# Kernel optimization log

Measured on AMD Instinct MI355X. Metric: run time of the kernel, lower is better.

The kernel has to match this reference:

```python
import jax, jax.numpy as jnp
import numpy as np

D = 512          # embedding_dim (cfg.hidden_size)
K = 1024         # codebook_size
DECAY = 0.99
EPS = 1e-05
COMMITMENT_COST = 0.25


def setup_inputs() -> dict:
    key = jax.random.key(0)
    k1, k2, k3 = jax.random.split(key, 3)
    return {
        "inputs": jax.random.normal(k1, (32, 1024, D), dtype=jnp.float32),
        "embedding_weight": jax.random.normal(k2, (K, D), dtype=jnp.float32),
        "ema_cluster_size": jnp.zeros((K,), dtype=jnp.float32),
        "ema_w": jax.random.normal(k3, (K, D), dtype=jnp.float32),
    }


def reference(inputs, embedding_weight, ema_cluster_size, ema_w):
    input_shape = inputs.shape
    flat = inputs.reshape(-1, D)  # [N, D]

    # Squared L2 distances to every codebook entry: [N, K]
    distances = (
        jnp.sum(flat ** 2, axis=1, keepdims=True)
        + jnp.sum(embedding_weight ** 2, axis=1)
        - 2.0 * flat @ embedding_weight.T
    )
    idx = jnp.argmin(distances, axis=1)                      # [N]
    encodings = jax.nn.one_hot(idx, K, dtype=flat.dtype)     # [N, K]

    # ---- EMA codebook update (training path) ----
    counts = jnp.sum(encodings, axis=0)                      # == bincount(idx)
    new_cs = ema_cluster_size * DECAY + (1.0 - DECAY) * counts
    n = jnp.sum(new_cs)
    new_cs = (new_cs + EPS) / (n + K * EPS) * n              # Laplace smoothing
    # dw = encodings.T @ flat, done as a fused gather-reduce instead of dense matmul
    dw = jax.ops.segment_sum(flat, idx, num_segments=K)      # [K, D]
    new_ema_w = ema_w * DECAY + (1.0 - DECAY) * dw
    new_embedding = new_ema_w / new_cs[:, None]              # updated codebook

    # quantized = encodings @ new_embedding, expressed as a gather
    quantized = new_embedding[idx].reshape(input_shape)

    e_latent_loss = jnp.mean((jax.lax.stop_gradient(quantized) - inputs) ** 2)
    loss = COMMITMENT_COST * e_latent_loss

    # straight-through estimator
    quantized = inputs + jax.lax.stop_gradient(quantized - inputs)

    avg_probs = jnp.mean(encodings, axis=0)
    perplexity = jnp.exp(-jnp.sum(avg_probs * jnp.log(avg_probs + 1e-10)))
    return (loss, quantized, perplexity, encodings)
```

## Files before the change

### kernel.cpp

```cpp
#include <hip/hip_runtime.h>

#define NROWS 32768
#define DIM   512
#define KC    1024

typedef __attribute__((ext_vector_type(8)))  short short8v;
typedef __attribute__((ext_vector_type(16))) float f32x16;

#define AS1 __attribute__((address_space(1)))
#define AS3 __attribute__((address_space(3)))

__global__ __launch_bounds__(256) void k_enorm(const float* __restrict__ E,
                                               float* __restrict__ en2) {
    int w = threadIdx.x >> 6, lane = threadIdx.x & 63;
    int c = blockIdx.x * 4 + w;
    const float* row = E + (size_t)c * DIM;
    float4 a = *reinterpret_cast<const float4*>(&row[lane * 8]);
    float4 b = *reinterpret_cast<const float4*>(&row[lane * 8 + 4]);
    float s = a.x*a.x + a.y*a.y + a.z*a.z + a.w*a.w
            + b.x*b.x + b.y*b.y + b.z*b.z + b.w*b.w;
    #pragma unroll
    for (int off = 32; off; off >>= 1) s += __shfl_xor(s, off);
    if (!lane) en2[c] = s;
}

__device__ __forceinline__ void split_bf16(float v, short& hi, short& lo) {
    unsigned u = __float_as_uint(v);
    unsigned r = u + 0x7FFFu + ((u >> 16) & 1u);
    hi = (short)(r >> 16);
    float hif = __uint_as_float(r & 0xFFFF0000u);
    float rem = v - hif;
    unsigned u2 = __float_as_uint(rem);
    unsigned r2 = u2 + 0x7FFFu + ((u2 >> 16) & 1u);
    lo = (short)(r2 >> 16);
}

__device__ __forceinline__ unsigned long long pack_key(float d, int c) {
    unsigned u = __float_as_uint(d);
    u = (u & 0x80000000u) ? ~u : (u | 0x80000000u);
    return ((unsigned long long)u << 32) | (unsigned)c;
}

__global__ __launch_bounds__(256) void k_split(const float* __restrict__ x,
                                               const float* __restrict__ E,
                                               short* __restrict__ xfrag,
                                               short* __restrict__ efrag,
                                               int* __restrict__ counts,
                                               unsigned long long* __restrict__ packed) {
    __shared__ short hbuf[32][520];
    __shared__ short lbuf[32][520];
    int b = blockIdx.x, t = threadIdx.x;
    const float* src;
    short* dst;
    if (b < NROWS / 32) {
        src = x + (size_t)b * 32 * DIM;
        dst = xfrag + (size_t)b * 32768;
        if (b == 0) {
            #pragma unroll
            for (int i = 0; i < 4; ++i) counts[t + i * 256] = 0;
        }
    } else {
        int eb = b - NROWS / 32;
        src = E + (size_t)eb * 32 * DIM;
        dst = efrag + (size_t)eb * 32768;
        unsigned long long* p = packed + eb * 1024;
        #pragma unroll
        for (int i = 0; i < 4; ++i) p[t + i * 256] = 0xFFFFFFFFFFFFFFFFull;
    }
    #pragma unroll
    for (int f = 0; f < 16; ++f) {
        int u = t + f * 256;
        int row = u >> 7, c4 = (u & 127) * 4;
        float4 v = *reinterpret_cast<const float4*>(&src[row * DIM + c4]);
        short4 h4, l4;
        split_bf16(v.x, h4.x, l4.x); split_bf16(v.y, h4.y, l4.y);
        split_bf16(v.z, h4.z, l4.z); split_bf16(v.w, h4.w, l4.w);
        *reinterpret_cast<short4*>(&hbuf[row][c4]) = h4;
        *reinterpret_cast<short4*>(&lbuf[row][c4]) = l4;
    }
    __syncthreads();
    #pragma unroll
    for (int f = 0; f < 16; ++f) {
        int u = t + f * 256;
        int lane = u & 63, h = (u >> 6) & 1, kb = u >> 7;
        int row = lane & 31, k0 = kb * 16 + (lane >> 5) * 8;
        const short* s = h ? &lbuf[row][k0] : &hbuf[row][k0];
        short8v val = *reinterpret_cast<const short8v*>(s);
        *reinterpret_cast<short8v*>(&dst[(size_t)u * 8]) = val;
    }
}

__global__ __launch_bounds__(256, 2) void k_argmin(const short* __restrict__ xfrag,
                                                   const short* __restrict__ efrag,
                                                   const float* __restrict__ en2,
                                                   unsigned long long* __restrict__ packed) {
    __shared__ short sbuf[3][12288];
    const int tid = threadIdx.x;
    const int w = tid >> 6, l = tid & 63;
    const int wr = w >> 1, wc = w & 1;
    const int l31 = l & 31, lh = l >> 5;

    int bid = blockIdx.x;
    int xcd = bid & 7, j = bid >> 3;
    int row0 = (xcd * 32 + (j >> 2)) * 128;
    int c0   = (j & 3) * 256;

    const short* gsrc[6];
    #pragma unroll
    for (int s = 0; s < 6; ++s) {
        int q = s * 4 + w, g = q >> 1, h = q & 1;
        const short* base = (g < 4)
            ? xfrag + (size_t)(row0 / 32 + g) * 32768
            : efrag + (size_t)(c0 / 32 + (g - 4)) * 32768;
        gsrc[s] = base + h * 512 + l * 8;
    }

    f32x16 acc[2][4];
    #pragma unroll
    for (int a = 0; a < 2; ++a)
        #pragma unroll
        for (int b = 0; b < 4; ++b)
            #pragma unroll
            for (int r = 0; r < 16; ++r) acc[a][b][r] = 0.f;

    #pragma unroll
    for (int s = 0; s < 6; ++s)
        __builtin_amdgcn_global_load_lds((const AS1 void*)gsrc[s],
                                         (AS3 void*)&sbuf[0][(s * 4 + w) * 512],
                                         16, 0, 0);
    #pragma unroll
    for (int s = 0; s < 6; ++s)
        __builtin_amdgcn_global_load_lds((const AS1 void*)(gsrc[s] + 1024),
                                         (AS3 void*)&sbuf[1][(s * 4 + w) * 512],
                                         16, 0, 0);
    asm volatile("s_waitcnt vmcnt(6)" ::: "memory");
    __builtin_amdgcn_s_barrier();

    #pragma unroll 3
    for (int kb = 0; kb < 30; ++kb) {
        const int cur = kb % 3, nxt = (kb + 2) % 3;
        #pragma unroll
        for (int s = 0; s < 6; ++s)
            __builtin_amdgcn_global_load_lds(
                (const AS1 void*)(gsrc[s] + (size_t)(kb + 2) * 1024),
                (AS3 void*)&sbuf[nxt][(s * 4 + w) * 512], 16, 0, 0);
        {
            short8v ah[2], al[2], bh[4], bl[4];
            const short* sb = sbuf[cur];
            #pragma unroll
            for (int m = 0; m < 2; ++m) {
                int g = wr * 2 + m;
                ah[m] = *reinterpret_cast<const short8v*>(&sb[(g * 2 + 0) * 512 + l * 8]);
                al[m] = *reinterpret_cast<const short8v*>(&sb[(g * 2 + 1) * 512 + l * 8]);
            }
            #pragma unroll
            for (int n = 0; n < 4; ++n) {
                int g = 4 + wc * 4 + n;
                bh[n] = *reinterpret_cast<const short8v*>(&sb[(g * 2 + 0) * 512 + l * 8]);
                bl[n] = *reinterpret_cast<const short8v*>(&sb[(g * 2 + 1) * 512 + l * 8]);
            }
            #pragma unroll
            for (int m = 0; m < 2; ++m)
                #pragma unroll
                for (int n = 0; n < 4; ++n) {
                    acc[m][n] = __builtin_amdgcn_mfma_f32_32x32x16_bf16(
                        ah[m], bh[n], acc[m][n], 0, 0, 0);
                    acc[m][n] = __builtin_amdgcn_mfma_f32_32x32x16_bf16(
                        ah[m], bl[n], acc[m][n], 0, 0, 0);
                    acc[m][n] = __builtin_amdgcn_mfma_f32_32x32x16_bf16(
                        al[m], bh[n], acc[m][n], 0, 0, 0);
                }
        }
        asm volatile("s_waitcnt vmcnt(6) lgkmcnt(0)" ::: "memory");
        __builtin_amdgcn_s_barrier();
    }

    #pragma unroll
    for (int e = 0; e < 2; ++e) {
        const int kb = 30 + e, cur = kb % 3;
        short8v ah[2], al[2], bh[4], bl[4];
        const short* sb = sbuf[cur];
        #pragma unroll
        for (int m = 0; m < 2; ++m) {
            int g = wr * 2 + m;
            ah[m] = *reinterpret_cast<const short8v*>(&sb[(g * 2 + 0) * 512 + l * 8]);
            al[m] = *reinterpret_cast<const short8v*>(&sb[(g * 2 + 1) * 512 + l * 8]);
        }
        #pragma unroll
        for (int n = 0; n < 4; ++n) {
            int g = 4 + wc * 4 + n;
            bh[n] = *reinterpret_cast<const short8v*>(&sb[(g * 2 + 0) * 512 + l * 8]);
            bl[n] = *reinterpret_cast<const short8v*>(&sb[(g * 2 + 1) * 512 + l * 8]);
        }
        #pragma unroll
        for (int m = 0; m < 2; ++m)
            #pragma unroll
            for (int n = 0; n < 4; ++n) {
                acc[m][n] = __builtin_amdgcn_mfma_f32_32x32x16_bf16(
                    ah[m], bh[n], acc[m][n], 0, 0, 0);
                acc[m][n] = __builtin_amdgcn_mfma_f32_32x32x16_bf16(
                    ah[m], bl[n], acc[m][n], 0, 0, 0);
                acc[m][n] = __builtin_amdgcn_mfma_f32_32x32x16_bf16(
                    al[m], bh[n], acc[m][n], 0, 0, 0);
            }
        if (e == 0) {
            asm volatile("s_waitcnt vmcnt(0) lgkmcnt(0)" ::: "memory");
            __builtin_amdgcn_s_barrier();
        }
    }

    float e2[4];
    #pragma unroll
    for (int n = 0; n < 4; ++n) e2[n] = en2[c0 + wc * 128 + n * 32 + l31];
    #pragma unroll
    for (int m = 0; m < 2; ++m) {
        #pragma unroll
        for (int r = 0; r < 16; ++r) {
            unsigned long long key = 0xFFFFFFFFFFFFFFFFull;
            #pragma unroll
            for (int n = 0; n < 4; ++n) {
                float d = fmaf(-2.f, acc[m][n][r], e2[n]);
                unsigned long long k = pack_key(d, c0 + wc * 128 + n * 32 + l31);
                if (k < key) key = k;
            }
            #pragma unroll
            for (int off = 1; off < 32; off <<= 1) {
                unsigned long long o = __shfl_xor(key, off);
                if (o < key) key = o;
            }
            if (l31 == 0) {
                int grow = row0 + wr * 64 + m * 32 + (r & 3) + 8 * (r >> 2) + 4 * lh;
                atomicMin(&packed[grow], key);
            }
        }
    }
}

__global__ __launch_bounds__(256) void k_hist(const unsigned long long* __restrict__ packed,
                                              int* __restrict__ idx,
                                              int* __restrict__ counts) {
    __shared__ int h[KC];
    for (int i = threadIdx.x; i < KC; i += 256) h[i] = 0;
    __syncthreads();
    int g = blockIdx.x * 256 + threadIdx.x;
    int c = (int)(unsigned)(packed[g] & 0xFFFFFFFFull);
    idx[g] = c;
    atomicAdd(&h[c], 1);
    __syncthreads();
    for (int i = threadIdx.x; i < KC; i += 256)
        if (h[i]) atomicAdd(&counts[i], h[i]);
}

__global__ __launch_bounds__(1024) void k_meta(const int* __restrict__ counts,
                                               const float* __restrict__ ema_cs,
                                               float* __restrict__ smoothed,
                                               int* __restrict__ offsets,
                                               int* __restrict__ cursor,
                                               float* __restrict__ perp_out) {
    __shared__ float ws1[16], ws2[16];
    __shared__ int wsum[16];
    int t = threadIdx.x, lane = t & 63, w = t >> 6;
    int cnt = counts[t];
    float cs = ema_cs[t] * 0.99f + 0.01f * (float)cnt;
    float p = (float)cnt / 32768.f;
    float v1 = cs, v2 = p * logf(p + 1e-10f);
    #pragma unroll
    for (int off = 32; off; off >>= 1) {
        v1 += __shfl_xor(v1, off);
        v2 += __shfl_xor(v2, off);
    }
    int s = cnt;
    #pragma unroll
    for (int off = 1; off < 64; off <<= 1) {
        int u = __shfl_up(s, off);
        if (lane >= off) s += u;
    }
    if (lane == 0) { ws1[w] = v1; ws2[w] = v2; }
    if (lane == 63) wsum[w] = s;
    __syncthreads();
    float n = 0.f;
    #pragma unroll
    for (int i = 0; i < 16; ++i) n += ws1[i];
    smoothed[t] = (cs + 1e-5f) / (n + 1024.f * 1e-5f) * n;
    if (t == 0) {
        float sp = 0.f;
        #pragma unroll
        for (int i = 0; i < 16; ++i) sp += ws2[i];
        perp_out[0] = expf(-sp);
    }
    int wo = 0;
    for (int i = 0; i < 16; ++i) if (i < w) wo += wsum[i];
    int off_ = wo + s - cnt;
    offsets[t] = off_;
    cursor[t] = off_;
}

__global__ __launch_bounds__(256) void k_scatter(const int* __restrict__ idx,
                                                 int* __restrict__ cursor,
                                                 int* __restrict__ bucket) {
    int g = blockIdx.x * 256 + threadIdx.x;
    int c = idx[g];
    int pos = atomicAdd(&cursor[c], 1);
    bucket[pos] = g;
}

__global__ __launch_bounds__(256) void k_dw(const float* __restrict__ x,
                                            const float* __restrict__ ema_w,
                                            const int* __restrict__ offsets,
                                            const int* __restrict__ counts,
                                            const int* __restrict__ bucket,
                                            const float* __restrict__ smoothed,
                                            float* __restrict__ newE) {
    __shared__ int rows[256];
    int k = blockIdx.x >> 1, half = blockIdx.x & 1, t = threadIdx.x;
    int d = half * 256 + t;
    int beg = offsets[k], m = counts[k];
    float a = 0.f;
    for (int base = 0; base < m; base += 256) {
        int n = min(256, m - base);
        __syncthreads();
        if (t < n) rows[t] = bucket[beg + base + t];
        __syncthreads();
        int i = 0;
        for (; i + 4 <= n; i += 4) {
            float v0 = x[(size_t)rows[i]     * DIM + d];
            float v1 = x[(size_t)rows[i + 1] * DIM + d];
            float v2 = x[(size_t)rows[i + 2] * DIM + d];
            float v3 = x[(size_t)rows[i + 3] * DIM + d];
            a += v0 + v1 + v2 + v3;
        }
        for (; i < n; ++i) a += x[(size_t)rows[i] * DIM + d];
    }
    newE[(size_t)k * DIM + d] =
        (ema_w[(size_t)k * DIM + d] * 0.99f + 0.01f * a) / smoothed[k];
}

__global__ __launch_bounds__(256) void k_qe(const float* __restrict__ x,
                                            const int* __restrict__ idx,
                                            const float* __restrict__ newE,
                                            float* __restrict__ outq,
                                            float* __restrict__ enc,
                                            float* __restrict__ partials) {
    int b = blockIdx.x, t = threadIdx.x;
    int row8 = b * 8;
    float lp = 0.f;
    #pragma unroll
    for (int it = 0; it < 4; ++it) {
        int slot = t + it * 256;
        int r = slot >> 7;
        int c4 = (slot & 127) * 4;
        int row = row8 + r;
        int code = idx[row];
        float4 in = *reinterpret_cast<const float4*>(&x[(size_t)row * DIM + c4]);
        float4 q  = *reinterpret_cast<const float4*>(&newE[(size_t)code * DIM + c4]);
        float4 d;
        d.x = q.x - in.x; d.y = q.y - in.y; d.z = q.z - in.z; d.w = q.w - in.w;
        float4 o;
        o.x = in.x + d.x; o.y = in.y + d.y; o.z = in.z + d.z; o.w = in.w + d.w;
        *reinterpret_cast<float4*>(&outq[(size_t)row * DIM + c4]) = o;
        lp += d.x*d.x + d.y*d.y + d.z*d.z + d.w*d.w;
    }
    {
        int er = row8 + (t >> 5);
        int l32 = t & 31;
        int one = idx[er];
        float4* dst = reinterpret_cast<float4*>(enc + (size_t)er * KC);
        #pragma unroll
        for (int s = 0; s < 8; ++s) {
            int c4 = l32 + s * 32;
            int base = c4 * 4;
            float4 v;
            v.x = (one == base)     ? 1.f : 0.f;
            v.y = (one == base + 1) ? 1.f : 0.f;
            v.z = (one == base + 2) ? 1.f : 0.f;
            v.w = (one == base + 3) ? 1.f : 0.f;
            dst[c4] = v;
        }
    }
    #pragma unroll
    for (int off = 32; off; off >>= 1) lp += __shfl_xor(lp, off);
    __shared__ float wr[4];
    int lane = t & 63, w = t >> 6;
    if (!lane) wr[w] = lp;
    __syncthreads();
    if (t == 0) partials[b] = wr[0] + wr[1] + wr[2] + wr[3];
}

__global__ __launch_bounds__(256) void k_lossfin(const float* __restrict__ partials,
                                                 float* __restrict__ out0) {
    __shared__ double red[256];
    double s = 0.0;
    for (int i = threadIdx.x; i < 4096; i += 256) s += (double)partials[i];
    red[threadIdx.x] = s; __syncthreads();
    for (int st = 128; st; st >>= 1) {
        if (threadIdx.x < st) red[threadIdx.x] += red[threadIdx.x + st];
        __syncthreads();
    }
    if (!threadIdx.x) out0[0] = (float)(0.25 * red[0] / 16777216.0);
}

extern "C" void kernel_launch(void* const* d_in, const int* in_sizes, int n_in,
                              void* d_out, int out_size, void* d_ws, size_t ws_size,
                              hipStream_t stream) {
    const float* x   = (const float*)d_in[0];
    const float* E   = (const float*)d_in[1];
    const float* ecs = (const float*)d_in[2];
    const float* emw = (const float*)d_in[3];
    float* out = (float*)d_out;

    char* ws = (char*)d_ws;
    int*   idx      = (int*)(ws + 0);
    int*   bucket   = (int*)(ws + 131072);
    float* en2      = (float*)(ws + 262144);
    int*   counts   = (int*)(ws + 266240);
    int*   offsets  = (int*)(ws + 270336);
    int*   cursor   = (int*)(ws + 274432);
    float* smoothed = (float*)(ws + 278528);
    float* newE     = (float*)(ws + 282624);
    float* partials = (float*)(ws + 282624 + 2097152);
    unsigned long long* packed = (unsigned long long*)newE;

    float* out_loss = out;
    float* out_q    = out + 1;
    float* out_perp = out + 16777217;
    float* out_enc  = out + 16777218;

    short* xfrag = (short*)out_enc;
    short* efrag = xfrag + (size_t)NROWS * DIM * 2;

    k_enorm  <<<KC / 4, 256, 0, stream>>>(E, en2);
    k_split  <<<NROWS / 32 + KC / 32, 256, 0, stream>>>(x, E, xfrag, efrag,
                                                        counts, packed);
    k_argmin <<<(NROWS / 128) * 4, 256, 0, stream>>>(xfrag, efrag, en2, packed);
    k_hist   <<<NROWS / 256, 256, 0, stream>>>(packed, idx, counts);
    k_meta   <<<1, 1024, 0, stream>>>(counts, ecs, smoothed, offsets, cursor, out_perp);
    k_scatter<<<NROWS / 256, 256, 0, stream>>>(idx, cursor, bucket);
    k_dw     <<<KC * 2, 256, 0, stream>>>(x, emw, offsets, counts, bucket, smoothed, newE);
    k_qe     <<<NROWS / 8, 256, 0, stream>>>(x, idx, newE, out_q, out_enc, partials);
    k_lossfin<<<1, 256, 0, stream>>>(partials, out_loss);
}
```

Before: 301.1 us.

## Fuse x bf16 split into argmin GEMM loop and merge E prep kernels

```diff
diff --git a/kernel.cpp b/kernel.cpp
--- a/kernel.cpp
+++ b/kernel.cpp
@@ -9,20 +9,6 @@
 
 #define AS1 __attribute__((address_space(1)))
 #define AS3 __attribute__((address_space(3)))
-
-__global__ __launch_bounds__(256) void k_enorm(const float* __restrict__ E,
-                                               float* __restrict__ en2) {
-    int w = threadIdx.x >> 6, lane = threadIdx.x & 63;
-    int c = blockIdx.x * 4 + w;
-    const float* row = E + (size_t)c * DIM;
-    float4 a = *reinterpret_cast<const float4*>(&row[lane * 8]);
-    float4 b = *reinterpret_cast<const float4*>(&row[lane * 8 + 4]);
-    float s = a.x*a.x + a.y*a.y + a.z*a.z + a.w*a.w
-            + b.x*b.x + b.y*b.y + b.z*b.z + b.w*b.w;
-    #pragma unroll
-    for (int off = 32; off; off >>= 1) s += __shfl_xor(s, off);
-    if (!lane) en2[c] = s;
-}
 
 __device__ __forceinline__ void split_bf16(float v, short& hi, short& lo) {
     unsigned u = __float_as_uint(v);
@@ -35,38 +21,44 @@
     lo = (short)(r2 >> 16);
 }
 
+__device__ __forceinline__ void conv8(const float4 a, const float4 b,
+                                      short8v& hi, short8v& lo) {
+    short h, l;
+    split_bf16(a.x, h, l); hi[0] = h; lo[0] = l;
+    split_bf16(a.y, h, l); hi[1] = h; lo[1] = l;
+    split_bf16(a.z, h, l); hi[2] = h; lo[2] = l;
+    split_bf16(a.w, h, l); hi[3] = h; lo[3] = l;
+    split_bf16(b.x, h, l); hi[4] = h; lo[4] = l;
+    split_bf16(b.y, h, l); hi[5] = h; lo[5] = l;
+    split_bf16(b.z, h, l); hi[6] = h; lo[6] = l;
+    split_bf16(b.w, h, l); hi[7] = h; lo[7] = l;
+}
+
 __device__ __forceinline__ unsigned long long pack_key(float d, int c) {
     unsigned u = __float_as_uint(d);
     u = (u & 0x80000000u) ? ~u : (u | 0x80000000u);
     return ((unsigned long long)u << 32) | (unsigned)c;
 }
 
-__global__ __launch_bounds__(256) void k_split(const float* __restrict__ x,
-                                               const float* __restrict__ E,
-                                               short* __restrict__ xfrag,
+__global__ __launch_bounds__(256) void k_eprep(const float* __restrict__ E,
                                                short* __restrict__ efrag,
+                                               float* __restrict__ en2,
                                                int* __restrict__ counts,
                                                unsigned long long* __restrict__ packed) {
     __shared__ short hbuf[32][520];
     __shared__ short lbuf[32][520];
     int b = blockIdx.x, t = threadIdx.x;
-    const float* src;
-    short* dst;
-    if (b < NROWS / 32) {
-        src = x + (size_t)b * 32 * DIM;
-        dst = xfrag + (size_t)b * 32768;
-        if (b == 0) {
-            #pragma unroll
-            for (int i = 0; i < 4; ++i) counts[t + i * 256] = 0;
-        }
-    } else {
-        int eb = b - NROWS / 32;
-        src = E + (size_t)eb * 32 * DIM;
-        dst = efrag + (size_t)eb * 32768;
-        unsigned long long* p = packed + eb * 1024;
-        #pragma unroll
-        for (int i = 0; i < 4; ++i) p[t + i * 256] = 0xFFFFFFFFFFFFFFFFull;
-    }
+    const float* src = E + (size_t)b * 32 * DIM;
+    short* dst = efrag + (size_t)b * 32768;
+
+    unsigned long long* p = packed + b * 1024;
+    #pragma unroll
+    for (int i = 0; i < 4; ++i) p[t + i * 256] = 0xFFFFFFFFFFFFFFFFull;
+    if (b == 0) {
+        #pragma unroll
+        for (int i = 0; i < 4; ++i) counts[t + i * 256] = 0;
+    }
+
     #pragma unroll
     for (int f = 0; f < 16; ++f) {
         int u = t + f * 256;
@@ -88,9 +80,22 @@
         short8v val = *reinterpret_cast<const short8v*>(s);
         *reinterpret_cast<short8v*>(&dst[(size_t)u * 8]) = val;
     }
-}
-
-__global__ __launch_bounds__(256, 2) void k_argmin(const short* __restrict__ xfrag,
+
+    int w = t >> 6, lane = t & 63;
+    for (int cc = 0; cc < 8; ++cc) {
+        int c = b * 32 + w * 8 + cc;
+        const float* row = E + (size_t)c * DIM;
+        float4 a = *reinterpret_cast<const float4*>(&row[lane * 8]);
+        float4 bb = *reinterpret_cast<const float4*>(&row[lane * 8 + 4]);
+        float s = a.x*a.x + a.y*a.y + a.z*a.z + a.w*a.w
+                + bb.x*bb.x + bb.y*bb.y + bb.z*bb.z + bb.w*bb.w;
+        #pragma unroll
+        for (int off = 32; off; off >>= 1) s += __shfl_xor(s, off);
+        if (!lane) en2[c] = s;
+    }
+}
+
+__global__ __launch_bounds__(256, 2) void k_argmin(const float* __restrict__ x,
                                                    const short* __restrict__ efrag,
                                                    const float* __restrict__ en2,
                                                    unsigned long long* __restrict__ packed) {
@@ -105,14 +110,12 @@
     int row0 = (xcd * 32 + (j >> 2)) * 128;
     int c0   = (j & 3) * 256;
 
-    const short* gsrc[6];
-    #pragma unroll
-    for (int s = 0; s < 6; ++s) {
-        int q = s * 4 + w, g = q >> 1, h = q & 1;
-        const short* base = (g < 4)
-            ? xfrag + (size_t)(row0 / 32 + g) * 32768
-            : efrag + (size_t)(c0 / 32 + (g - 4)) * 32768;
-        gsrc[s] = base + h * 512 + l * 8;
+    const float* axsrc = x + (size_t)(row0 + w * 32 + l31) * DIM + lh * 8;
+    const short* gsrc[4];
+    #pragma unroll
+    for (int s = 0; s < 4; ++s) {
+        int gb = w * 2 + (s >> 1), h = s & 1;
+        gsrc[s] = efrag + (size_t)(c0 / 32 + gb) * 32768 + h * 512 + l * 8;
     }
 
     f32x16 acc[2][4];
@@ -123,27 +126,47 @@
             #pragma unroll
             for (int r = 0; r < 16; ++r) acc[a][b][r] = 0.f;
 
-    #pragma unroll
-    for (int s = 0; s < 6; ++s)
+    float4 a00 = *reinterpret_cast<const float4*>(axsrc);
+    float4 a01 = *reinterpret_cast<const float4*>(axsrc + 4);
+    __builtin_amdgcn_sched_barrier(0);
+    #pragma unroll
+    for (int s = 0; s < 4; ++s)
         __builtin_amdgcn_global_load_lds((const AS1 void*)gsrc[s],
-                                         (AS3 void*)&sbuf[0][(s * 4 + w) * 512],
+                                         (AS3 void*)&sbuf[0][(8 + w * 4 + s) * 512],
                                          16, 0, 0);
-    #pragma unroll
-    for (int s = 0; s < 6; ++s)
+    __builtin_amdgcn_sched_barrier(0);
+    float4 a10 = *reinterpret_cast<const float4*>(axsrc + 16);
+    float4 a11 = *reinterpret_cast<const float4*>(axsrc + 20);
+    __builtin_amdgcn_sched_barrier(0);
+    #pragma unroll
+    for (int s = 0; s < 4; ++s)
         __builtin_amdgcn_global_load_lds((const AS1 void*)(gsrc[s] + 1024),
-                                         (AS3 void*)&sbuf[1][(s * 4 + w) * 512],
+                                         (AS3 void*)&sbuf[1][(8 + w * 4 + s) * 512],
                                          16, 0, 0);
-    asm volatile("s_waitcnt vmcnt(6)" ::: "memory");
-    __builtin_amdgcn_s_barrier();
+    {
+        asm volatile("s_waitcnt vmcnt(10)" ::: "memory");
+        short8v hi, lo; conv8(a00, a01, hi, lo);
+        *reinterpret_cast<short8v*>(&sbuf[0][(w * 2 + 0) * 512 + l * 8]) = hi;
+        *reinterpret_cast<short8v*>(&sbuf[0][(w * 2 + 1) * 512 + l * 8]) = lo;
+        asm volatile("s_waitcnt vmcnt(4)" ::: "memory");
+        conv8(a10, a11, hi, lo);
+        *reinterpret_cast<short8v*>(&sbuf[1][(w * 2 + 0) * 512 + l * 8]) = hi;
+        *reinterpret_cast<short8v*>(&sbuf[1][(w * 2 + 1) * 512 + l * 8]) = lo;
+        asm volatile("s_waitcnt lgkmcnt(0)" ::: "memory");
+        __builtin_amdgcn_s_barrier();
+    }
 
     #pragma unroll 3
     for (int kb = 0; kb < 30; ++kb) {
         const int cur = kb % 3, nxt = (kb + 2) % 3;
-        #pragma unroll
-        for (int s = 0; s < 6; ++s)
+        float4 an0 = *reinterpret_cast<const float4*>(axsrc + (kb + 2) * 16);
+        float4 an1 = *reinterpret_cast<const float4*>(axsrc + (kb + 2) * 16 + 4);
+        __builtin_amdgcn_sched_barrier(0);
+        #pragma unroll
+        for (int s = 0; s < 4; ++s)
             __builtin_amdgcn_global_load_lds(
                 (const AS1 void*)(gsrc[s] + (size_t)(kb + 2) * 1024),
-                (AS3 void*)&sbuf[nxt][(s * 4 + w) * 512], 16, 0, 0);
+                (AS3 void*)&sbuf[nxt][(8 + w * 4 + s) * 512], 16, 0, 0);
         {
             short8v ah[2], al[2], bh[4], bl[4];
             const short* sb = sbuf[cur];
@@ -171,7 +194,13 @@
                         al[m], bh[n], acc[m][n], 0, 0, 0);
                 }
         }
-        asm volatile("s_waitcnt vmcnt(6) lgkmcnt(0)" ::: "memory");
+        asm volatile("s_waitcnt vmcnt(4)" ::: "memory");
+        {
+            short8v hi, lo; conv8(an0, an1, hi, lo);
+            *reinterpret_cast<short8v*>(&sbuf[nxt][(w * 2 + 0) * 512 + l * 8]) = hi;
+            *reinterpret_cast<short8v*>(&sbuf[nxt][(w * 2 + 1) * 512 + l * 8]) = lo;
+        }
+        asm volatile("s_waitcnt lgkmcnt(0)" ::: "memory");
         __builtin_amdgcn_s_barrier();
     }
 
@@ -425,13 +454,10 @@
     float* out_perp = out + 16777217;
     float* out_enc  = out + 16777218;
 
-    short* xfrag = (short*)out_enc;
-    short* efrag = xfrag + (size_t)NROWS * DIM * 2;
-
-    k_enorm  <<<KC / 4, 256, 0, stream>>>(E, en2);
-    k_split  <<<NROWS / 32 + KC / 32, 256, 0, stream>>>(x, E, xfrag, efrag,
-                                                        counts, packed);
-    k_argmin <<<(NROWS / 128) * 4, 256, 0, stream>>>(xfrag, efrag, en2, packed);
+    short* efrag = (short*)out_enc;
+
+    k_eprep  <<<KC / 32, 256, 0, stream>>>(E, efrag, en2, counts, packed);
+    k_argmin <<<(NROWS / 128) * 4, 256, 0, stream>>>(x, efrag, en2, packed);
     k_hist   <<<NROWS / 256, 256, 0, stream>>>(packed, idx, counts);
     k_meta   <<<1, 1024, 0, stream>>>(counts, ecs, smoothed, offsets, cursor, out_perp);
     k_scatter<<<NROWS / 256, 256, 0, stream>>>(idx, cursor, bucket);
```

Result: faster. 292.4 us (-2.9%).
